# Optimization experiments

Measured on AMD Instinct MI355X. Metric: run time of the kernel, lower is better.

The kernel has to match this reference:

```python
import jax, jax.numpy as jnp
import numpy as np

H_IMG = 1024
W_IMG = 1024


def _create_meshgrid(height, width):
    # normalized coordinates in [-1, 1], shape [height, width, 2] as (x, y)
    xs = jnp.linspace(-1.0, 1.0, width, dtype=jnp.float32)
    ys = jnp.linspace(-1.0, 1.0, height, dtype=jnp.float32)
    gx, gy = jnp.meshgrid(xs, ys)  # [H, W] each
    return jnp.stack([gx, gy], axis=-1)  # [H, W, 2]


def _warp_grid(homo, height, width):
    # homo: [N, 3, 3]; returns flow [N, H, W, 2] in normalized coords
    grid = _create_meshgrid(height, width)  # [H, W, 2]
    ones = jnp.ones(grid.shape[:-1] + (1,), dtype=grid.dtype)
    pts = jnp.concatenate([grid, ones], axis=-1)  # [H, W, 3]
    # transformed homogeneous points: [N, H, W, 3]
    warped = jnp.einsum('nij,hwj->nhwi', homo, pts)
    return warped[..., :2] / warped[..., 2:3]


def _grid_sample_bilinear_zeros(img, flow):
    # img: [N, C, H, W]; flow: [N, Ho, Wo, 2] normalized (x, y) in [-1, 1]
    # align_corners=True semantics (torch default pre-1.3 / tgm era)
    N, C, H, W = img.shape
    x = (flow[..., 0] + 1.0) * 0.5 * (W - 1)  # [N, Ho, Wo]
    y = (flow[..., 1] + 1.0) * 0.5 * (H - 1)

    x0 = jnp.floor(x)
    y0 = jnp.floor(y)
    x1 = x0 + 1.0
    y1 = y0 + 1.0

    wx1 = x - x0
    wx0 = 1.0 - wx1
    wy1 = y - y0
    wy0 = 1.0 - wy1

    img_flat = img.reshape(N, C, H * W)

    def gather(ix, iy):
        # zeros padding: mask out-of-bounds corners, clip indices for gather
        valid = ((ix >= 0) & (ix <= W - 1) & (iy >= 0) & (iy <= H - 1))
        ixc = jnp.clip(ix, 0, W - 1).astype(jnp.int32)
        iyc = jnp.clip(iy, 0, H - 1).astype(jnp.int32)
        lin = (iyc * W + ixc).reshape(N, 1, -1)  # [N, 1, Ho*Wo]
        vals = jnp.take_along_axis(img_flat, lin, axis=2)  # [N, C, Ho*Wo]
        vals = vals.reshape(N, C, *ix.shape[1:])
        return vals * valid[:, None].astype(img.dtype)

    out = (gather(x0, y0) * (wx0 * wy0)[:, None]
           + gather(x1, y0) * (wx1 * wy0)[:, None]
           + gather(x0, y1) * (wx0 * wy1)[:, None]
           + gather(x1, y1) * (wx1 * wy1)[:, None])
    return out


def setup_inputs() -> dict:
    key = jax.random.key(0)
    k1, k2 = jax.random.split(key)
    patch_src = jax.random.normal(k1, (16, 3, H_IMG, W_IMG), dtype=jnp.float32)
    # identity homography plus small perturbation (realistic warp, mostly in-bounds)
    eye = jnp.eye(3, dtype=jnp.float32)[None]
    noise = 0.05 * jax.random.normal(k2, (16, 3, 3), dtype=jnp.float32)
    dst_homo_src = eye + noise
    return {"patch_src": patch_src, "dst_homo_src": dst_homo_src}


def reference(patch_src, dst_homo_src):
    flow = _warp_grid(dst_homo_src, H_IMG, W_IMG)  # [N, H, W, 2]
    return _grid_sample_bilinear_zeros(patch_src, flow)
```

## Files before the change

kernel.cpp:

```cpp
#include <hip/hip_runtime.h>

#define H_IMG 1024
#define W_IMG 1024
#define N_IMG 16
#define C_IMG 3

__global__ __launch_bounds__(256) void homography_warp_kernel(
    const float* __restrict__ img,
    const float* __restrict__ homo,
    float* __restrict__ out)
{
    const int n   = blockIdx.y;
    const int pix = blockIdx.x * 256 + threadIdx.x;
    const int h   = pix >> 10;
    const int w   = pix & (W_IMG - 1);

    const float* Hm = homo + n * 9;
    const float h00 = Hm[0], h01 = Hm[1], h02 = Hm[2];
    const float h10 = Hm[3], h11 = Hm[4], h12 = Hm[5];
    const float h20 = Hm[6], h21 = Hm[7], h22 = Hm[8];

    const float gx = fmaf((float)w, 2.0f / (W_IMG - 1), -1.0f);
    const float gy = fmaf((float)h, 2.0f / (H_IMG - 1), -1.0f);

    const float tx = fmaf(h00, gx, fmaf(h01, gy, h02));
    const float ty = fmaf(h10, gx, fmaf(h11, gy, h12));
    const float tz = fmaf(h20, gx, fmaf(h21, gy, h22));
    const float inv = 1.0f / tz;
    const float u = tx * inv;
    const float v = ty * inv;

    const float xp = (u + 1.0f) * 0.5f * (float)(W_IMG - 1);
    const float yp = (v + 1.0f) * 0.5f * (float)(H_IMG - 1);

    const float x0f = floorf(xp);
    const float y0f = floorf(yp);
    const float fx = xp - x0f;
    const float fy = yp - y0f;

    const int ix0 = (int)x0f;
    const int iy0 = (int)y0f;
    const int ix1 = ix0 + 1;
    const int iy1 = iy0 + 1;

    const float vx0 = (ix0 >= 0 && ix0 < W_IMG) ? 1.0f : 0.0f;
    const float vx1 = (ix1 >= 0 && ix1 < W_IMG) ? 1.0f : 0.0f;
    const float vy0 = (iy0 >= 0 && iy0 < H_IMG) ? 1.0f : 0.0f;
    const float vy1 = (iy1 >= 0 && iy1 < H_IMG) ? 1.0f : 0.0f;

    const float w00 = (1.0f - fx) * (1.0f - fy) * vx0 * vy0;
    const float w01 = fx * (1.0f - fy) * vx1 * vy0;
    const float w10 = (1.0f - fx) * fy * vx0 * vy1;
    const float w11 = fx * fy * vx1 * vy1;

    const int cx0 = min(max(ix0, 0), W_IMG - 1);
    const int cx1 = min(max(ix1, 0), W_IMG - 1);
    const int cy0 = min(max(iy0, 0), H_IMG - 1);
    const int cy1 = min(max(iy1, 0), H_IMG - 1);

    const int o00 = cy0 * W_IMG + cx0;
    const int o01 = cy0 * W_IMG + cx1;
    const int o10 = cy1 * W_IMG + cx0;
    const int o11 = cy1 * W_IMG + cx1;

    const size_t plane = (size_t)H_IMG * W_IMG;
    const size_t base  = (size_t)n * C_IMG * plane;

#pragma unroll
    for (int c = 0; c < C_IMG; ++c) {
        const float* p = img + base + (size_t)c * plane;
        const float r = w00 * p[o00] + w01 * p[o01] + w10 * p[o10] + w11 * p[o11];
        out[base + (size_t)c * plane + (size_t)pix] = r;
    }
}

extern "C" void kernel_launch(void* const* d_in, const int* in_sizes, int n_in,
                              void* d_out, int out_size, void* d_ws, size_t ws_size,
                              hipStream_t stream) {
    const float* img  = (const float*)d_in[0];
    const float* homo = (const float*)d_in[1];
    float* out = (float*)d_out;

    dim3 block(256);
    dim3 grid((H_IMG * W_IMG) / 256, N_IMG);
    homography_warp_kernel<<<grid, block, 0, stream>>>(img, homo, out);
}
```

Measured before the change: 376.5 us.

## Stage warped source footprint in shared memory per 2D output tile

Each block now covers a 32x16 output tile. It maps the tile corners through the homography to get a bounding box of the source region, and when that box fits in 48x32 it cooperatively loads all three channels into LDS. The bilinear gathers are then served from LDS, with a fallback to direct global gathers when the box is too large. A block-index swizzle changes the order tiles are scheduled in, and the division uses a fast reciprocal with one Newton step. This adds LDS traffic, a barrier and some redundant loads in exchange for coalesced loads and reuse of source pixels.

Result: slower. 425.2 us (+12.9%).

```diff
diff --git a/kernel.cpp b/kernel.cpp
--- a/kernel.cpp
+++ b/kernel.cpp
@@ -5,72 +5,153 @@
 #define N_IMG 16
 #define C_IMG 3
 
+#define TW 32
+#define TH 16
+#define LX 48
+#define LY 32
+
 __global__ __launch_bounds__(256) void homography_warp_kernel(
     const float* __restrict__ img,
     const float* __restrict__ homo,
     float* __restrict__ out)
 {
+    __shared__ float smem[C_IMG][LY][LX];
+
     const int n   = blockIdx.y;
-    const int pix = blockIdx.x * 256 + threadIdx.x;
-    const int h   = pix >> 10;
-    const int w   = pix & (W_IMG - 1);
+    const int pbx = blockIdx.x;
+    const int lbx = (pbx & 7) * (2048 / 8) + (pbx >> 3);
+    const int tile_r = lbx >> 5;
+    const int tile_c = lbx & 31;
+    const int c0 = tile_c * TW;
+    const int r0 = tile_r * TH;
+
+    const int tid  = threadIdx.x;
+    const int col  = c0 + (tid & 31);
+    const int row0 = r0 + (tid >> 5);
 
     const float* Hm = homo + n * 9;
     const float h00 = Hm[0], h01 = Hm[1], h02 = Hm[2];
     const float h10 = Hm[3], h11 = Hm[4], h12 = Hm[5];
     const float h20 = Hm[6], h21 = Hm[7], h22 = Hm[8];
 
-    const float gx = fmaf((float)w, 2.0f / (W_IMG - 1), -1.0f);
-    const float gy = fmaf((float)h, 2.0f / (H_IMG - 1), -1.0f);
-
-    const float tx = fmaf(h00, gx, fmaf(h01, gy, h02));
-    const float ty = fmaf(h10, gx, fmaf(h11, gy, h12));
-    const float tz = fmaf(h20, gx, fmaf(h21, gy, h22));
-    const float inv = 1.0f / tz;
-    const float u = tx * inv;
-    const float v = ty * inv;
-
-    const float xp = (u + 1.0f) * 0.5f * (float)(W_IMG - 1);
-    const float yp = (v + 1.0f) * 0.5f * (float)(H_IMG - 1);
-
-    const float x0f = floorf(xp);
-    const float y0f = floorf(yp);
-    const float fx = xp - x0f;
-    const float fy = yp - y0f;
-
-    const int ix0 = (int)x0f;
-    const int iy0 = (int)y0f;
-    const int ix1 = ix0 + 1;
-    const int iy1 = iy0 + 1;
-
-    const float vx0 = (ix0 >= 0 && ix0 < W_IMG) ? 1.0f : 0.0f;
-    const float vx1 = (ix1 >= 0 && ix1 < W_IMG) ? 1.0f : 0.0f;
-    const float vy0 = (iy0 >= 0 && iy0 < H_IMG) ? 1.0f : 0.0f;
-    const float vy1 = (iy1 >= 0 && iy1 < H_IMG) ? 1.0f : 0.0f;
-
-    const float w00 = (1.0f - fx) * (1.0f - fy) * vx0 * vy0;
-    const float w01 = fx * (1.0f - fy) * vx1 * vy0;
-    const float w10 = (1.0f - fx) * fy * vx0 * vy1;
-    const float w11 = fx * fy * vx1 * vy1;
-
-    const int cx0 = min(max(ix0, 0), W_IMG - 1);
-    const int cx1 = min(max(ix1, 0), W_IMG - 1);
-    const int cy0 = min(max(iy0, 0), H_IMG - 1);
-    const int cy1 = min(max(iy1, 0), H_IMG - 1);
-
-    const int o00 = cy0 * W_IMG + cx0;
-    const int o01 = cy0 * W_IMG + cx1;
-    const int o10 = cy1 * W_IMG + cx0;
-    const int o11 = cy1 * W_IMG + cx1;
-
     const size_t plane = (size_t)H_IMG * W_IMG;
     const size_t base  = (size_t)n * C_IMG * plane;
 
+    float xmn = 1e30f, xmx = -1e30f, ymn = 1e30f, ymx = -1e30f;
 #pragma unroll
-    for (int c = 0; c < C_IMG; ++c) {
-        const float* p = img + base + (size_t)c * plane;
-        const float r = w00 * p[o00] + w01 * p[o01] + w10 * p[o10] + w11 * p[o11];
-        out[base + (size_t)c * plane + (size_t)pix] = r;
+    for (int k = 0; k < 4; ++k) {
+        const float gxc = fmaf((float)((k & 1) ? (c0 + TW - 1) : c0), 2.0f / (W_IMG - 1), -1.0f);
+        const float gyc = fmaf((float)((k & 2) ? (r0 + TH - 1) : r0), 2.0f / (H_IMG - 1), -1.0f);
+        const float txc = fmaf(h00, gxc, fmaf(h01, gyc, h02));
+        const float tyc = fmaf(h10, gxc, fmaf(h11, gyc, h12));
+        const float tzc = fmaf(h20, gxc, fmaf(h21, gyc, h22));
+        float ivc = __builtin_amdgcn_rcpf(tzc);
+        ivc = ivc * (2.0f - tzc * ivc);
+        const float xc = (txc * ivc + 1.0f) * 0.5f * (float)(W_IMG - 1);
+        const float yc = (tyc * ivc + 1.0f) * 0.5f * (float)(H_IMG - 1);
+        xmn = fminf(xmn, xc); xmx = fmaxf(xmx, xc);
+        ymn = fminf(ymn, yc); ymx = fmaxf(ymx, yc);
+    }
+    const int xmin = (int)floorf(xmn - 1.0f);
+    const int xmax = (int)floorf(xmx + 1.0f);
+    const int ymin = (int)floorf(ymn - 1.0f);
+    const int ymax = (int)floorf(ymx + 1.0f);
+
+    const int sx0 = min(max(xmin, 0), W_IMG - 2);
+    const int sx1 = min(max(xmax + 1, sx0 + 1), W_IMG - 1);
+    const int sy0 = min(max(ymin, 0), H_IMG - 1);
+    const int sy1 = min(max(ymax + 1, sy0), H_IMG - 1);
+    const int spanx = sx1 - sx0 + 1;
+    const int spany = sy1 - sy0 + 1;
+
+    const bool fast = (spanx <= LX) && (spany <= LY);
+
+    if (fast) {
+        const int total = spany * LX;
+#pragma unroll
+        for (int ch = 0; ch < C_IMG; ++ch) {
+            const float* pc = img + base + (size_t)ch * plane;
+            for (int i = tid; i < total; i += 256) {
+                const int ly = i / LX;
+                const int lx = i - ly * LX;
+                if (lx < spanx)
+                    smem[ch][ly][lx] = pc[(sy0 + ly) * W_IMG + sx0 + lx];
+            }
+        }
+        __syncthreads();
+    }
+
+#pragma unroll
+    for (int g = 0; g < 2; ++g) {
+        const int row = row0 + g * (TH / 2);
+        const int pix = row * W_IMG + col;
+
+        const float gx = fmaf((float)col, 2.0f / (W_IMG - 1), -1.0f);
+        const float gy = fmaf((float)row, 2.0f / (H_IMG - 1), -1.0f);
+
+        const float tx = fmaf(h00, gx, fmaf(h01, gy, h02));
+        const float ty = fmaf(h10, gx, fmaf(h11, gy, h12));
+        const float tz = fmaf(h20, gx, fmaf(h21, gy, h22));
+        float inv = __builtin_amdgcn_rcpf(tz);
+        inv = inv * (2.0f - tz * inv);
+        const float u = tx * inv;
+        const float v = ty * inv;
+
+        const float xp = (u + 1.0f) * 0.5f * (float)(W_IMG - 1);
+        const float yp = (v + 1.0f) * 0.5f * (float)(H_IMG - 1);
+
+        const float x0f = floorf(xp);
+        const float y0f = floorf(yp);
+        const float fx = xp - x0f;
+        const float fy = yp - y0f;
+
+        const int ix0 = (int)x0f;
+        const int iy0 = (int)y0f;
+        const int ix1 = ix0 + 1;
+        const int iy1 = iy0 + 1;
+
+        const float vx0 = (ix0 >= 0 && ix0 < W_IMG) ? 1.0f : 0.0f;
+        const float vx1 = (ix1 >= 0 && ix1 < W_IMG) ? 1.0f : 0.0f;
+        const float vy0 = (iy0 >= 0 && iy0 < H_IMG) ? 1.0f : 0.0f;
+        const float vy1 = (iy1 >= 0 && iy1 < H_IMG) ? 1.0f : 0.0f;
+
+        const float w00 = (1.0f - fx) * (1.0f - fy) * vx0 * vy0;
+        const float w01 = fx * (1.0f - fy) * vx1 * vy0;
+        const float w10 = (1.0f - fx) * fy * vx0 * vy1;
+        const float w11 = fx * fy * vx1 * vy1;
+
+        const int cx0 = min(max(ix0, 0), W_IMG - 1);
+        const int cx1 = min(max(ix1, 0), W_IMG - 1);
+        const int cy0 = min(max(iy0, 0), H_IMG - 1);
+        const int cy1 = min(max(iy1, 0), H_IMG - 1);
+
+        float r[C_IMG];
+        if (fast) {
+            const int lx0 = cx0 - sx0, lx1 = cx1 - sx0;
+            const int ly0 = cy0 - sy0, ly1 = cy1 - sy0;
+#pragma unroll
+            for (int ch = 0; ch < C_IMG; ++ch) {
+                const float v00 = smem[ch][ly0][lx0];
+                const float v01 = smem[ch][ly0][lx1];
+                const float v10 = smem[ch][ly1][lx0];
+                const float v11 = smem[ch][ly1][lx1];
+                r[ch] = w00 * v00 + w01 * v01 + w10 * v10 + w11 * v11;
+            }
+        } else {
+            const int o00 = cy0 * W_IMG + cx0;
+            const int o01 = cy0 * W_IMG + cx1;
+            const int o10 = cy1 * W_IMG + cx0;
+            const int o11 = cy1 * W_IMG + cx1;
+#pragma unroll
+            for (int ch = 0; ch < C_IMG; ++ch) {
+                const float* p = img + base + (size_t)ch * plane;
+                r[ch] = w00 * p[o00] + w01 * p[o01] + w10 * p[o10] + w11 * p[o11];
+            }
+        }
+
+#pragma unroll
+        for (int ch = 0; ch < C_IMG; ++ch)
+            out[base + (size_t)ch * plane + (size_t)pix] = r[ch];
     }
 }
 
@@ -82,6 +163,6 @@
     float* out = (float*)d_out;
 
     dim3 block(256);
-    dim3 grid((H_IMG * W_IMG) / 256, N_IMG);
+    dim3 grid((W_IMG / TW) * (H_IMG / TH), N_IMG);
     homography_warp_kernel<<<grid, block, 0, stream>>>(img, homo, out);
 }
```
